# Optimization experiments

Measured on AMD Instinct MI355X. Metric: run time of the kernel, lower is better.

Reference implementation:

```python
import jax, jax.numpy as jnp
import numpy as np

B, C, H, W = 2, 3, 256, 256
K_STEPS = 50
RHO = 0.5
SIGMA_INIT = float(0.5 / np.sqrt(2.0 * C))  # sigma_init == tau_init = 0.5/sqrt(C*2)


def nabla(x):
    # forward finite differences, zero at last row/col. x: [B,C,H,W] -> [B,C,2,H,W]
    dh = jnp.pad(x[:, :, 1:, :] - x[:, :, :-1, :], ((0, 0), (0, 0), (0, 1), (0, 0)))
    dw = jnp.pad(x[:, :, :, 1:] - x[:, :, :, :-1], ((0, 0), (0, 0), (0, 0), (0, 1)))
    return jnp.stack([dh, dw], axis=2)


def nablaT(u):
    # adjoint of nabla (negative divergence). u: [B,C,2,H,W] -> [B,C,H,W]
    v0, v1 = u[:, :, 0], u[:, :, 1]
    out = jnp.zeros(v0.shape, v0.dtype)
    out = out.at[:, :, 1:, :].add(v0[:, :, :-1, :]).at[:, :, :-1, :].add(-v0[:, :, :-1, :])
    out = out.at[:, :, :, 1:].add(v1[:, :, :, :-1]).at[:, :, :, :-1].add(-v1[:, :, :, :-1])
    return out


def l12_prox_conjugate(v, lamb):
    # Moreau: prox_{sigma*(lamb*f)*}(v) = v - sigma*prox_{(lamb/sigma) f}(v/sigma)
    # which for L12 reduces to projection onto the lamb-ball per group.
    # groups: l2 over axes (1,-2,-1) = (C,H,W), one group per (B, F).
    norm = jnp.sqrt(jnp.sum(v * v, axis=(1, 3, 4), keepdims=True))
    scale = lamb / jnp.maximum(norm, lamb)  # == min(1, lamb/norm), safe at 0
    return v * scale


def l2_prox(z, y, gamma):
    # argmin_u 0.5||u-z||^2 + gamma*0.5||u-y||^2  (A = identity)
    return (z + gamma * y) / (1.0 + gamma)


def setup_inputs() -> dict:
    key = jax.random.key(0)
    y = jax.random.normal(key, (B, C, H, W), dtype=jnp.float32)
    lambd = jnp.float32(-1.0)  # learnable scalar log-regularization weight
    return {"y": y, "lambd": lambd}


def reference(y, lambd):
    elambda = jnp.exp(lambd)
    # set_init: A_dagger = identity
    x0 = y
    xt0 = jnp.zeros_like(x0)
    u0 = nabla(x0)

    def step(carry, _):
        x, xt, u, sigma, tau = carry
        u_next = l12_prox_conjugate(u + sigma * nabla(xt), elambda)
        x_next = l2_prox(x - tau * nablaT(u_next), y, tau)
        chi = 1.0 / jnp.sqrt(1.0 + 2.0 * RHO * tau)
        tau_next = tau * chi
        sigma_next = sigma / chi
        xt_next = (1.0 + chi) * x_next - chi * x
        return (x_next, xt_next, u_next, sigma_next, tau_next), None

    init = (x0, xt0, u0, jnp.float32(SIGMA_INIT), jnp.float32(SIGMA_INIT))
    (x, xt, u, _, _), _ = jax.lax.scan(step, init, None, length=K_STEPS)
    return (x, xt, u)
```

## Files before the change

### kernel.cpp

```cpp
#include <hip/hip_runtime.h>
#include <math.h>

constexpr int Cc = 3, Hh = 256;
constexpr int NX = 393216;
constexpr int R = 8;
constexpr int NBLK = 192;
constexpr int KSTEPS = 50;
constexpr int ROWQ = 128;
constexpr int BROWS = 12;
constexpr int SLOTQ = NBLK * BROWS * ROWQ;

using u64 = unsigned long long;
constexpr u64 SENT = 0x8000000080000000ull;

__device__ __forceinline__ float4 ld4(const float* p, int i) { return ((const float4*)p)[i]; }
__device__ __forceinline__ void st4(float* p, int i, float4 v) { ((float4*)p)[i] = v; }
__device__ __forceinline__ float4 mk4(float a, float b, float c, float d) { return make_float4(a, b, c, d); }
__device__ __forceinline__ u64 ldq(const u64* p) {
    return __hip_atomic_load(p, __ATOMIC_RELAXED, __HIP_MEMORY_SCOPE_AGENT);
}
__device__ __forceinline__ void stq(u64* p, u64 v) {
    __hip_atomic_store(p, v, __ATOMIC_RELAXED, __HIP_MEMORY_SCOPE_AGENT);
}
__device__ __forceinline__ void pub4(u64* w, float4 v) {
    union { float f[2]; u64 q; } a, b;
    a.f[0] = v.x; a.f[1] = v.y; b.f[0] = v.z; b.f[1] = v.w;
    stq(w, a.q); stq(w + 1, b.q);
}
__device__ __forceinline__ float4 unp(u64 lo, u64 hi) {
    union { u64 q; float f[2]; } a, b; a.q = lo; b.q = hi;
    return make_float4(a.f[0], a.f[1], b.f[0], b.f[1]);
}
__device__ __forceinline__ float4 col3(float4 P, float4 A, float4 B, float a, float b) {
    return mk4(fmaf(a, A.x, fmaf(b, B.x, P.x)), fmaf(a, A.y, fmaf(b, B.y, P.y)),
               fmaf(a, A.z, fmaf(b, B.z, P.z)), fmaf(a, A.w, fmaf(b, B.w, P.w)));
}
__device__ __forceinline__ float4 f4sub(float4 a, float4 b) {
    return mk4(a.x - b.x, a.y - b.y, a.z - b.z, a.w - b.w);
}
__device__ __forceinline__ float4 f4s(float4 a, float s) {
    return mk4(a.x * s, a.y * s, a.z * s, a.w * s);
}
__device__ __forceinline__ float4 f4fma(float s, float4 a, float4 b) {
    return mk4(fmaf(s, a.x, b.x), fmaf(s, a.y, b.y), fmaf(s, a.z, b.z), fmaf(s, a.w, b.w));
}
__device__ __forceinline__ float4 nth(float4 vm, bool up, float4 v0x, bool dn) {
    return mk4((up ? vm.x : 0.f) - (dn ? v0x.x : 0.f), (up ? vm.y : 0.f) - (dn ? v0x.y : 0.f),
               (up ? vm.z : 0.f) - (dn ? v0x.z : 0.f), (up ? vm.w : 0.f) - (dn ? v0x.w : 0.f));
}
__device__ __forceinline__ float4 ntw(float4 v1x, int c4) {
    float ul = __shfl_up(v1x.w, 1, 64);
    return mk4(((c4 > 0) ? ul : 0.f) - v1x.x, v1x.x - v1x.y, v1x.y - v1x.z,
               v1x.z - ((c4 < 63) ? v1x.w : 0.f));
}
__device__ __forceinline__ float4 gradw(float4 t, int c4) {
    float xn = __shfl_down(t.x, 1, 64);
    return mk4(t.y - t.x, t.z - t.y, t.w - t.z, (c4 < 63) ? (xn - t.w) : 0.f);
}
__device__ __forceinline__ void barld() {
    asm volatile("s_waitcnt lgkmcnt(0)" ::: "memory");
    __builtin_amdgcn_sched_barrier(0);
    __builtin_amdgcn_s_barrier();
    __builtin_amdgcn_sched_barrier(0);
}

__global__ void init_ws(u64* h0, u64* h1, u64* h2, u64* parts) {
    int i = blockIdx.x * 256 + threadIdx.x;
    if (i < SLOTQ) { h0[i] = SENT; h1[i] = SENT; h2[i] = SENT; }
    if (i < (KSTEPS + 1) * NBLK) parts[i] = SENT;
}

__global__ void __launch_bounds__(512, 1) cp_persist(
    const float* __restrict__ y, const float* __restrict__ lambd,
    float* __restrict__ xout, float* __restrict__ xtout, float* __restrict__ uout,
    u64* __restrict__ h0, u64* __restrict__ h1, u64* __restrict__ h2,
    u64* __restrict__ parts)
{
    __shared__ float sv0[8 * 256];
    __shared__ float sxtP[9 * 256];
    __shared__ float sxtA[9 * 256];
    __shared__ float sxtB[9 * 256];
    __shared__ float2 pw[8];

    const int tid = threadIdx.x, blk = blockIdx.x;
    const int bc = blk >> 5, tile = blk & 31, r0 = tile * R;
    const int c4 = tid & 63, trow = tid >> 6;
    const int b = (bc >= Cc) ? 1 : 0;
    const float lamb = expf(lambd[0]);
    const int gh = r0 + trow;
    const int j4 = bc * 16384 + gh * 64 + c4;

    float4 yv, xcur, v0c, v1c;
    float4 xpP, xpA, xpB, p0P, p0A, p0B, p1P, p1A, p1B;
    float4 yh = mk4(0, 0, 0, 0), vmtop = yh, v0h = yh, v1h = yh, xoh = yh;

    float tau = 0.20412414523193150818f;
    float sig = tau;
    float chi = 0.f, sigs = 0.f;
    float alpha = 0.f, beta = 0.f;

    auto slotp = [&](int r) -> u64* { return (r == 0) ? h0 : ((r == 1) ? h1 : h2); };

    auto wavesum2 = [&](float& a, float& bb) {
        #pragma unroll
        for (int m = 1; m < 64; m <<= 1) { a += __shfl_xor(a, m, 64); bb += __shfl_xor(bb, m, 64); }
    };

    auto pollscale = [&](int s) {
        const u64* pb = parts + (size_t)s * NBLK + b * 96;
        const int i1 = 64 + (c4 & 31);
        u64 q0, q1;
        for (;;) {
            q0 = ldq(pb + c4);
            q1 = ldq(pb + i1);
            if (__all((q0 != SENT) && (q1 != SENT))) break;
            __builtin_amdgcn_s_sleep(1);
        }
        asm volatile("" ::: "memory");
        union { u64 q; float f[2]; } a;
        a.q = q0;
        float g0 = a.f[0], g1 = a.f[1];
        a.q = q1;
        if (c4 < 32) { g0 += a.f[0]; g1 += a.f[1]; }
        wavesum2(g0, g1);
        alpha = lamb / fmaxf(sqrtf(g0), lamb);
        beta  = lamb / fmaxf(sqrtf(g1), lamb);
    };

    auto wavenorm = [&]() {
        float pa0 = v0c.x*v0c.x + v0c.y*v0c.y + v0c.z*v0c.z + v0c.w*v0c.w;
        float pa1 = v1c.x*v1c.x + v1c.y*v1c.y + v1c.z*v1c.z + v1c.w*v1c.w;
        wavesum2(pa0, pa1);
        if (c4 == 0) pw[trow] = make_float2(pa0, pa1);
    };
    auto pubparts = [&](int s) {
        if (tid == 0) {
            float q0 = 0.f, q1 = 0.f;
            #pragma unroll
            for (int w = 0; w < 8; ++w) { q0 += pw[w].x; q1 += pw[w].y; }
            union { float f[2]; u64 q; } pk; pk.f[0] = q0; pk.f[1] = q1;
            stq(parts + (size_t)s * NBLK + blk, pk.q);
        }
    };

    auto expand = [&](u64* hb, bool pub) {
        const float inv = 1.f / (1.f + tau);
        const float tin = tau * inv;
        const float opc = 1.f + chi;
        float4 xtP, xtA, xtB;
        {
            float4 vm = (trow > 0) ? ((float4*)(sv0 + (trow - 1) * 256))[c4] : vmtop;
            float4 NT0 = nth(vm, gh > 0, v0c, gh < Hh - 1);
            float4 NT1 = ntw(v1c, c4);
            float4 BASE = f4s(f4fma(tau, yv, xcur), inv);
            float4 xA = f4s(NT0, -tin);
            float4 xB = f4s(NT1, -tin);
            xpP = BASE; xpA = xA; xpB = xB;
            xtP = f4fma(-chi, xcur, f4s(BASE, opc));
            xtA = f4s(xA, opc);
            xtB = f4s(xB, opc);
            if (trow >= 1) {
                ((float4*)(sxtP + trow * 256))[c4] = xtP;
                ((float4*)(sxtA + trow * 256))[c4] = xtA;
                ((float4*)(sxtB + trow * 256))[c4] = xtB;
            }
            if (pub && trow == 0) {
                u64* rbase = hb + ((size_t)blk * BROWS) * ROWQ;
                pub4(rbase +  9 * ROWQ + 2 * c4, BASE);
                pub4(rbase + 10 * ROWQ + 2 * c4, xA);
                pub4(rbase + 11 * ROWQ + 2 * c4, xB);
            }
        }
        if (trow == 0 && tile < 31) {
            float4 vmh = ((float4*)(sv0 + 7 * 256))[c4];
            float4 NT0h = nth(vmh, true, v0h, true);
            float4 NT1h = ntw(v1h, c4);
            float4 BASEh = f4s(f4fma(tau, yh, xoh), inv);
            float4 xAh = f4s(NT0h, -tin);
            float4 xBh = f4s(NT1h, -tin);
            ((float4*)(sxtP + 8 * 256))[c4] = f4fma(-chi, xoh, f4s(BASEh, opc));
            ((float4*)(sxtA + 8 * 256))[c4] = f4s(xAh, opc);
            ((float4*)(sxtB + 8 * 256))[c4] = f4s(xBh, opc);
        }
        barld();
        {
            float4 dhP = mk4(0, 0, 0, 0), dhA = dhP, dhB = dhP;
            if (gh < Hh - 1) {
                dhP = f4sub(((float4*)(sxtP + (trow + 1) * 256))[c4], xtP);
                dhA = f4sub(((float4*)(sxtA + (trow + 1) * 256))[c4], xtA);
                dhB = f4sub(((float4*)(sxtB + (trow + 1) * 256))[c4], xtB);
            }
            float4 dwP = gradw(xtP, c4);
            float4 dwA = gradw(xtA, c4);
            float4 dwB = gradw(xtB, c4);
            p0P = f4s(dhP, sigs);
            p0A = f4fma(sigs, dhA, v0c);
            p0B = f4s(dhB, sigs);
            p1P = f4s(dwP, sigs);
            p1A = f4s(dwA, sigs);
            p1B = f4fma(sigs, dwB, v1c);
            if (pub) {
                u64* rbase = hb + ((size_t)blk * BROWS) * ROWQ;
                if (trow == 0) {
                    pub4(rbase + 3 * ROWQ + 2 * c4, p0P);
                    pub4(rbase + 4 * ROWQ + 2 * c4, p0A);
                    pub4(rbase + 5 * ROWQ + 2 * c4, p0B);
                    pub4(rbase + 6 * ROWQ + 2 * c4, p1P);
                    pub4(rbase + 7 * ROWQ + 2 * c4, p1A);
                    pub4(rbase + 8 * ROWQ + 2 * c4, p1B);
                }
                if (trow == 7) {
                    pub4(rbase + 0 * ROWQ + 2 * c4, p0P);
                    pub4(rbase + 1 * ROWQ + 2 * c4, p0A);
                    pub4(rbase + 2 * ROWQ + 2 * c4, p0B);
                }
            }
        }
        barld();
    };

    {
        yv = ld4(y, j4);
        xcur = yv;
        float4 dh = mk4(0, 0, 0, 0);
        if (gh < Hh - 1) dh = f4sub(ld4(y, j4 + 64), yv);
        v0c = dh;
        v1c = gradw(yv, c4);
        ((float4*)(sv0 + trow * 256))[c4] = v0c;
        if (trow == 0) {
            if (tile < 31) {
                const int j4h = bc * 16384 + (r0 + 8) * 64 + c4;
                yh = ld4(y, j4h);
                v0h = f4sub(ld4(y, j4h + 64), yh);
                v1h = gradw(yh, c4);
                xoh = yh;
            }
            if (tile > 0) {
                float4 ym = ld4(y, bc * 16384 + (r0 - 1) * 64 + c4);
                vmtop = f4sub(yv, ym);
            }
        }
        wavenorm();
        barld();
        pubparts(1);
        chi = 1.f / sqrtf(1.f + tau);
        sigs = sig / chi;
        expand(slotp(0), true);
        tau *= chi; sig = sigs;
    }

    for (int s = 1; s < KSTEPS; ++s) {
        pollscale(s);
        chi = 1.f / sqrtf(1.f + tau);
        sigs = sig / chi;

        xcur = col3(xpP, xpA, xpB, alpha, beta);
        v0c  = col3(p0P, p0A, p0B, alpha, beta);
        v1c  = col3(p1P, p1A, p1B, alpha, beta);
        ((float4*)(sv0 + trow * 256))[c4] = v0c;

        u64* hbp = slotp((s - 1) % 3);
        if (trow == 0) {
            if (tile > 0) {
                const u64* ra = hbp + ((size_t)(blk - 1) * BROWS) * ROWQ + 2 * c4;
                u64 a0, a1, a2, a3, a4, a5;
                for (;;) {
                    a0 = ldq(ra);            a1 = ldq(ra + 1);
                    a2 = ldq(ra + ROWQ);     a3 = ldq(ra + ROWQ + 1);
                    a4 = ldq(ra + 2 * ROWQ); a5 = ldq(ra + 2 * ROWQ + 1);
                    if (__all((a0 != SENT) && (a1 != SENT) && (a2 != SENT) &&
                              (a3 != SENT) && (a4 != SENT) && (a5 != SENT))) break;
                    __builtin_amdgcn_s_sleep(1);
                }
                vmtop = col3(unp(a0, a1), unp(a2, a3), unp(a4, a5), alpha, beta);
            }
            if (tile < 31) {
                const u64* rb = hbp + ((size_t)(blk + 1) * BROWS) * ROWQ + 2 * c4;
                u64 b0, b1, b2, b3, b4, b5, b6, b7, b8, b9, b10, b11, b12, b13, b14, b15, b16, b17;
                for (;;) {
                    b0  = ldq(rb + 3 * ROWQ);  b1  = ldq(rb + 3 * ROWQ + 1);
                    b2  = ldq(rb + 4 * ROWQ);  b3  = ldq(rb + 4 * ROWQ + 1);
                    b4  = ldq(rb + 5 * ROWQ);  b5  = ldq(rb + 5 * ROWQ + 1);
                    b6  = ldq(rb + 6 * ROWQ);  b7  = ldq(rb + 6 * ROWQ + 1);
                    b8  = ldq(rb + 7 * ROWQ);  b9  = ldq(rb + 7 * ROWQ + 1);
                    b10 = ldq(rb + 8 * ROWQ);  b11 = ldq(rb + 8 * ROWQ + 1);
                    b12 = ldq(rb + 9 * ROWQ);  b13 = ldq(rb + 9 * ROWQ + 1);
                    b14 = ldq(rb + 10 * ROWQ); b15 = ldq(rb + 10 * ROWQ + 1);
                    b16 = ldq(rb + 11 * ROWQ); b17 = ldq(rb + 11 * ROWQ + 1);
                    bool ok = (b0 != SENT) && (b1 != SENT) && (b2 != SENT) && (b3 != SENT) &&
                              (b4 != SENT) && (b5 != SENT) && (b6 != SENT) && (b7 != SENT) &&
                              (b8 != SENT) && (b9 != SENT) && (b10 != SENT) && (b11 != SENT) &&
                              (b12 != SENT) && (b13 != SENT) && (b14 != SENT) && (b15 != SENT) &&
                              (b16 != SENT) && (b17 != SENT);
                    if (__all(ok)) break;
                    __builtin_amdgcn_s_sleep(1);
                }
                v0h = col3(unp(b0, b1),   unp(b2, b3),   unp(b4, b5),   alpha, beta);
                v1h = col3(unp(b6, b7),   unp(b8, b9),   unp(b10, b11), alpha, beta);
                xoh = col3(unp(b12, b13), unp(b14, b15), unp(b16, b17), alpha, beta);
            }
        }
        asm volatile("" ::: "memory");

        if (s <= 47) {
            u64* rb2 = slotp((s + 1) % 3) + ((size_t)blk * BROWS) * ROWQ;
            if (trow == 0) {
                #pragma unroll
                for (int r = 3; r < 12; ++r) {
                    stq(rb2 + r * ROWQ + 2 * c4, SENT);
                    stq(rb2 + r * ROWQ + 2 * c4 + 1, SENT);
                }
            } else if (trow == 7) {
                #pragma unroll
                for (int r = 0; r < 3; ++r) {
                    stq(rb2 + r * ROWQ + 2 * c4, SENT);
                    stq(rb2 + r * ROWQ + 2 * c4 + 1, SENT);
                }
            }
        }
        wavenorm();
        barld();
        pubparts(s + 1);
        expand(slotp(s % 3), s < KSTEPS - 1);
        tau *= chi; sig = sigs;
    }

    pollscale(KSTEPS);
    const float opc = 1.f + chi;
    const int iv4 = bc * 32768 + gh * 64 + c4;
    float4 xf_ = col3(xpP, xpA, xpB, alpha, beta);
    float4 xtf = f4fma(-chi, xcur, f4s(xf_, opc));
    st4(xout, j4, xf_);
    st4(xtout, j4, xtf);
    st4(uout, iv4, f4s(v0c, alpha));
    st4(uout, iv4 + 16384, f4s(v1c, beta));
}

extern "C" void kernel_launch(void* const* d_in, const int* in_sizes, int n_in,
                              void* d_out, int out_size, void* d_ws, size_t ws_size,
                              hipStream_t stream) {
    (void)in_sizes; (void)n_in; (void)out_size; (void)ws_size;
    const float* y     = (const float*)d_in[0];
    const float* lambd = (const float*)d_in[1];
    float* xout  = (float*)d_out;
    float* xtout = xout + NX;
    float* uout  = xout + 2 * NX;

    u64* h0 = (u64*)d_out;
    u64* h1 = h0 + SLOTQ;
    u64* h2 = (u64*)d_ws;
    u64* parts = h2 + SLOTQ;

    init_ws<<<SLOTQ / 256, 256, 0, stream>>>(h0, h1, h2, parts);
    cp_persist<<<NBLK, 512, 0, stream>>>(y, lambd, xout, xtout, uout, h0, h1, h2, parts);
}
```

Before: 208.5 us.

## Move parts and halo polling to end of step and peel final iteration

Waiting for the global norm partials and for neighbour halos now happens at the end of each step, right after expand, instead of at the start of the next step. Only the halo-reading wave polls for halos, and the other waves can clear the next slot's sentinels before the norm-dependent scaling. The last step is peeled so the final expand skips the gradient and publish work that nothing reads, and it computes the outputs directly. This reorders cross-block synchronisation within the persistent kernel, which risks changing stall behaviour and correctness subtleties.

```diff
diff --git a/kernel.cpp b/kernel.cpp
--- a/kernel.cpp
+++ b/kernel.cpp
@@ -57,6 +57,9 @@
     float xn = __shfl_down(t.x, 1, 64);
     return mk4(t.y - t.x, t.z - t.y, t.w - t.z, (c4 < 63) ? (xn - t.w) : 0.f);
 }
+__device__ __forceinline__ float dot4(float4 a, float4 b) {
+    return a.x * b.x + a.y * b.y + a.z * b.z + a.w * b.w;
+}
 __device__ __forceinline__ void barld() {
     asm volatile("s_waitcnt lgkmcnt(0)" ::: "memory");
     __builtin_amdgcn_sched_barrier(0);
@@ -77,9 +80,7 @@
     u64* __restrict__ parts)
 {
     __shared__ float sv0[8 * 256];
-    __shared__ float sxtP[9 * 256];
-    __shared__ float sxtA[9 * 256];
-    __shared__ float sxtB[9 * 256];
+    __shared__ float sxtP[9 * 256], sxtA[9 * 256], sxtB[9 * 256];
     __shared__ float2 pw[8];
 
     const int tid = threadIdx.x, blk = blockIdx.x;
@@ -93,20 +94,16 @@
     float4 yv, xcur, v0c, v1c;
     float4 xpP, xpA, xpB, p0P, p0A, p0B, p1P, p1A, p1B;
     float4 yh = mk4(0, 0, 0, 0), vmtop = yh, v0h = yh, v1h = yh, xoh = yh;
-
-    float tau = 0.20412414523193150818f;
-    float sig = tau;
-    float chi = 0.f, sigs = 0.f;
-    float alpha = 0.f, beta = 0.f;
+    float tau = 0.20412414523193150818f, sig = tau, chi = 0.f, sigs = 0.f;
+    float g0 = 0.f, g1 = 0.f;
 
     auto slotp = [&](int r) -> u64* { return (r == 0) ? h0 : ((r == 1) ? h1 : h2); };
-
     auto wavesum2 = [&](float& a, float& bb) {
         #pragma unroll
         for (int m = 1; m < 64; m <<= 1) { a += __shfl_xor(a, m, 64); bb += __shfl_xor(bb, m, 64); }
     };
 
-    auto pollscale = [&](int s) {
+    auto pollparts = [&](int s) {
         const u64* pb = parts + (size_t)s * NBLK + b * 96;
         const int i1 = 64 + (c4 & 31);
         u64 q0, q1;
@@ -119,17 +116,55 @@
         asm volatile("" ::: "memory");
         union { u64 q; float f[2]; } a;
         a.q = q0;
-        float g0 = a.f[0], g1 = a.f[1];
+        g0 = a.f[0]; g1 = a.f[1];
         a.q = q1;
         if (c4 < 32) { g0 += a.f[0]; g1 += a.f[1]; }
         wavesum2(g0, g1);
-        alpha = lamb / fmaxf(sqrtf(g0), lamb);
-        beta  = lamb / fmaxf(sqrtf(g1), lamb);
-    };
-
+    };
+    auto halopoll = [&](int sl, float al, float be) {
+        u64* hbp = slotp(sl);
+        if (tile > 0) {
+            const u64* ra = hbp + ((size_t)(blk - 1) * BROWS) * ROWQ + 2 * c4;
+            u64 a0, a1, a2, a3, a4, a5;
+            for (;;) {
+                a0 = ldq(ra);            a1 = ldq(ra + 1);
+                a2 = ldq(ra + ROWQ);     a3 = ldq(ra + ROWQ + 1);
+                a4 = ldq(ra + 2 * ROWQ); a5 = ldq(ra + 2 * ROWQ + 1);
+                if (__all((a0 != SENT) && (a1 != SENT) && (a2 != SENT) &&
+                          (a3 != SENT) && (a4 != SENT) && (a5 != SENT))) break;
+                __builtin_amdgcn_s_sleep(1);
+            }
+            vmtop = col3(unp(a0, a1), unp(a2, a3), unp(a4, a5), al, be);
+        } else vmtop = mk4(0, 0, 0, 0);
+        if (tile < 31) {
+            const u64* rb = hbp + ((size_t)(blk + 1) * BROWS) * ROWQ + 2 * c4;
+            u64 b0, b1, b2, b3, b4, b5, b6, b7, b8, b9, b10, b11, b12, b13, b14, b15, b16, b17;
+            for (;;) {
+                b0  = ldq(rb + 3 * ROWQ);  b1  = ldq(rb + 3 * ROWQ + 1);
+                b2  = ldq(rb + 4 * ROWQ);  b3  = ldq(rb + 4 * ROWQ + 1);
+                b4  = ldq(rb + 5 * ROWQ);  b5  = ldq(rb + 5 * ROWQ + 1);
+                b6  = ldq(rb + 6 * ROWQ);  b7  = ldq(rb + 6 * ROWQ + 1);
+                b8  = ldq(rb + 7 * ROWQ);  b9  = ldq(rb + 7 * ROWQ + 1);
+                b10 = ldq(rb + 8 * ROWQ);  b11 = ldq(rb + 8 * ROWQ + 1);
+                b12 = ldq(rb + 9 * ROWQ);  b13 = ldq(rb + 9 * ROWQ + 1);
+                b14 = ldq(rb + 10 * ROWQ); b15 = ldq(rb + 10 * ROWQ + 1);
+                b16 = ldq(rb + 11 * ROWQ); b17 = ldq(rb + 11 * ROWQ + 1);
+                bool ok = (b0 != SENT) && (b1 != SENT) && (b2 != SENT) && (b3 != SENT) &&
+                          (b4 != SENT) && (b5 != SENT) && (b6 != SENT) && (b7 != SENT) &&
+                          (b8 != SENT) && (b9 != SENT) && (b10 != SENT) && (b11 != SENT) &&
+                          (b12 != SENT) && (b13 != SENT) && (b14 != SENT) && (b15 != SENT) &&
+                          (b16 != SENT) && (b17 != SENT);
+                if (__all(ok)) break;
+                __builtin_amdgcn_s_sleep(1);
+            }
+            v0h = col3(unp(b0, b1),   unp(b2, b3),   unp(b4, b5),   al, be);
+            v1h = col3(unp(b6, b7),   unp(b8, b9),   unp(b10, b11), al, be);
+            xoh = col3(unp(b12, b13), unp(b14, b15), unp(b16, b17), al, be);
+        }
+        asm volatile("" ::: "memory");
+    };
     auto wavenorm = [&]() {
-        float pa0 = v0c.x*v0c.x + v0c.y*v0c.y + v0c.z*v0c.z + v0c.w*v0c.w;
-        float pa1 = v1c.x*v1c.x + v1c.y*v1c.y + v1c.z*v1c.z + v1c.w*v1c.w;
+        float pa0 = dot4(v0c, v0c), pa1 = dot4(v1c, v1c);
         wavesum2(pa0, pa1);
         if (c4 == 0) pw[trow] = make_float2(pa0, pa1);
     };
@@ -142,19 +177,15 @@
             stq(parts + (size_t)s * NBLK + blk, pk.q);
         }
     };
-
     auto expand = [&](u64* hb, bool pub) {
-        const float inv = 1.f / (1.f + tau);
-        const float tin = tau * inv;
-        const float opc = 1.f + chi;
+        const float inv = 1.f / (1.f + tau), tin = tau * inv, opc = 1.f + chi;
         float4 xtP, xtA, xtB;
         {
             float4 vm = (trow > 0) ? ((float4*)(sv0 + (trow - 1) * 256))[c4] : vmtop;
             float4 NT0 = nth(vm, gh > 0, v0c, gh < Hh - 1);
             float4 NT1 = ntw(v1c, c4);
             float4 BASE = f4s(f4fma(tau, yv, xcur), inv);
-            float4 xA = f4s(NT0, -tin);
-            float4 xB = f4s(NT1, -tin);
+            float4 xA = f4s(NT0, -tin), xB = f4s(NT1, -tin);
             xpP = BASE; xpA = xA; xpB = xB;
             xtP = f4fma(-chi, xcur, f4s(BASE, opc));
             xtA = f4s(xA, opc);
@@ -176,44 +207,33 @@
             float4 NT0h = nth(vmh, true, v0h, true);
             float4 NT1h = ntw(v1h, c4);
             float4 BASEh = f4s(f4fma(tau, yh, xoh), inv);
-            float4 xAh = f4s(NT0h, -tin);
-            float4 xBh = f4s(NT1h, -tin);
             ((float4*)(sxtP + 8 * 256))[c4] = f4fma(-chi, xoh, f4s(BASEh, opc));
-            ((float4*)(sxtA + 8 * 256))[c4] = f4s(xAh, opc);
-            ((float4*)(sxtB + 8 * 256))[c4] = f4s(xBh, opc);
-        }
-        barld();
-        {
-            float4 dhP = mk4(0, 0, 0, 0), dhA = dhP, dhB = dhP;
-            if (gh < Hh - 1) {
-                dhP = f4sub(((float4*)(sxtP + (trow + 1) * 256))[c4], xtP);
-                dhA = f4sub(((float4*)(sxtA + (trow + 1) * 256))[c4], xtA);
-                dhB = f4sub(((float4*)(sxtB + (trow + 1) * 256))[c4], xtB);
-            }
-            float4 dwP = gradw(xtP, c4);
-            float4 dwA = gradw(xtA, c4);
-            float4 dwB = gradw(xtB, c4);
-            p0P = f4s(dhP, sigs);
-            p0A = f4fma(sigs, dhA, v0c);
-            p0B = f4s(dhB, sigs);
-            p1P = f4s(dwP, sigs);
-            p1A = f4s(dwA, sigs);
-            p1B = f4fma(sigs, dwB, v1c);
-            if (pub) {
-                u64* rbase = hb + ((size_t)blk * BROWS) * ROWQ;
-                if (trow == 0) {
-                    pub4(rbase + 3 * ROWQ + 2 * c4, p0P);
-                    pub4(rbase + 4 * ROWQ + 2 * c4, p0A);
-                    pub4(rbase + 5 * ROWQ + 2 * c4, p0B);
-                    pub4(rbase + 6 * ROWQ + 2 * c4, p1P);
-                    pub4(rbase + 7 * ROWQ + 2 * c4, p1A);
-                    pub4(rbase + 8 * ROWQ + 2 * c4, p1B);
-                }
-                if (trow == 7) {
-                    pub4(rbase + 0 * ROWQ + 2 * c4, p0P);
-                    pub4(rbase + 1 * ROWQ + 2 * c4, p0A);
-                    pub4(rbase + 2 * ROWQ + 2 * c4, p0B);
-                }
+            ((float4*)(sxtA + 8 * 256))[c4] = f4s(f4s(NT0h, -tin), opc);
+            ((float4*)(sxtB + 8 * 256))[c4] = f4s(f4s(NT1h, -tin), opc);
+        }
+        barld();
+        float4 dhP = mk4(0, 0, 0, 0), dhA = dhP, dhB = dhP;
+        if (gh < Hh - 1) {
+            dhP = f4sub(((float4*)(sxtP + (trow + 1) * 256))[c4], xtP);
+            dhA = f4sub(((float4*)(sxtA + (trow + 1) * 256))[c4], xtA);
+            dhB = f4sub(((float4*)(sxtB + (trow + 1) * 256))[c4], xtB);
+        }
+        float4 dwP = gradw(xtP, c4), dwA = gradw(xtA, c4), dwB = gradw(xtB, c4);
+        p0P = f4s(dhP, sigs); p0A = f4fma(sigs, dhA, v0c); p0B = f4s(dhB, sigs);
+        p1P = f4s(dwP, sigs); p1A = f4s(dwA, sigs); p1B = f4fma(sigs, dwB, v1c);
+        if (pub) {
+            u64* rbase = hb + ((size_t)blk * BROWS) * ROWQ;
+            if (trow == 0) {
+                pub4(rbase + 3 * ROWQ + 2 * c4, p0P);
+                pub4(rbase + 4 * ROWQ + 2 * c4, p0A);
+                pub4(rbase + 5 * ROWQ + 2 * c4, p0B);
+                pub4(rbase + 6 * ROWQ + 2 * c4, p1P);
+                pub4(rbase + 7 * ROWQ + 2 * c4, p1A);
+                pub4(rbase + 8 * ROWQ + 2 * c4, p1B);
+            } else if (trow == 7) {
+                pub4(rbase + 0 * ROWQ + 2 * c4, p0P);
+                pub4(rbase + 1 * ROWQ + 2 * c4, p0A);
+                pub4(rbase + 2 * ROWQ + 2 * c4, p0B);
             }
         }
         barld();
@@ -222,9 +242,7 @@
     {
         yv = ld4(y, j4);
         xcur = yv;
-        float4 dh = mk4(0, 0, 0, 0);
-        if (gh < Hh - 1) dh = f4sub(ld4(y, j4 + 64), yv);
-        v0c = dh;
+        v0c = (gh < Hh - 1) ? f4sub(ld4(y, j4 + 64), yv) : mk4(0, 0, 0, 0);
         v1c = gradw(yv, c4);
         ((float4*)(sv0 + trow * 256))[c4] = v0c;
         if (trow == 0) {
@@ -241,68 +259,26 @@
             }
         }
         wavenorm();
-        barld();
-        pubparts(1);
         chi = 1.f / sqrtf(1.f + tau);
         sigs = sig / chi;
+        barld();
+        pubparts(1);
         expand(slotp(0), true);
+        pollparts(1);
+        if (trow == 0) {
+            float al = lamb / fmaxf(sqrtf(g0), lamb);
+            float be = lamb / fmaxf(sqrtf(g1), lamb);
+            halopoll(0, al, be);
+        }
         tau *= chi; sig = sigs;
     }
 
-    for (int s = 1; s < KSTEPS; ++s) {
-        pollscale(s);
+    for (int s = 1; s < KSTEPS - 1; ++s) {
+        const float al = lamb / fmaxf(sqrtf(g0), lamb);
+        const float be = lamb / fmaxf(sqrtf(g1), lamb);
         chi = 1.f / sqrtf(1.f + tau);
         sigs = sig / chi;
-
-        xcur = col3(xpP, xpA, xpB, alpha, beta);
-        v0c  = col3(p0P, p0A, p0B, alpha, beta);
-        v1c  = col3(p1P, p1A, p1B, alpha, beta);
-        ((float4*)(sv0 + trow * 256))[c4] = v0c;
-
-        u64* hbp = slotp((s - 1) % 3);
-        if (trow == 0) {
-            if (tile > 0) {
-                const u64* ra = hbp + ((size_t)(blk - 1) * BROWS) * ROWQ + 2 * c4;
-                u64 a0, a1, a2, a3, a4, a5;
-                for (;;) {
-                    a0 = ldq(ra);            a1 = ldq(ra + 1);
-                    a2 = ldq(ra + ROWQ);     a3 = ldq(ra + ROWQ + 1);
-                    a4 = ldq(ra + 2 * ROWQ); a5 = ldq(ra + 2 * ROWQ + 1);
-                    if (__all((a0 != SENT) && (a1 != SENT) && (a2 != SENT) &&
-                              (a3 != SENT) && (a4 != SENT) && (a5 != SENT))) break;
-                    __builtin_amdgcn_s_sleep(1);
-                }
-                vmtop = col3(unp(a0, a1), unp(a2, a3), unp(a4, a5), alpha, beta);
-            }
-            if (tile < 31) {
-                const u64* rb = hbp + ((size_t)(blk + 1) * BROWS) * ROWQ + 2 * c4;
-                u64 b0, b1, b2, b3, b4, b5, b6, b7, b8, b9, b10, b11, b12, b13, b14, b15, b16, b17;
-                for (;;) {
-                    b0  = ldq(rb + 3 * ROWQ);  b1  = ldq(rb + 3 * ROWQ + 1);
-                    b2  = ldq(rb + 4 * ROWQ);  b3  = ldq(rb + 4 * ROWQ + 1);
-                    b4  = ldq(rb + 5 * ROWQ);  b5  = ldq(rb + 5 * ROWQ + 1);
-                    b6  = ldq(rb + 6 * ROWQ);  b7  = ldq(rb + 6 * ROWQ + 1);
-                    b8  = ldq(rb + 7 * ROWQ);  b9  = ldq(rb + 7 * ROWQ + 1);
-                    b10 = ldq(rb + 8 * ROWQ);  b11 = ldq(rb + 8 * ROWQ + 1);
-                    b12 = ldq(rb + 9 * ROWQ);  b13 = ldq(rb + 9 * ROWQ + 1);
-                    b14 = ldq(rb + 10 * ROWQ); b15 = ldq(rb + 10 * ROWQ + 1);
-                    b16 = ldq(rb + 11 * ROWQ); b17 = ldq(rb + 11 * ROWQ + 1);
-                    bool ok = (b0 != SENT) && (b1 != SENT) && (b2 != SENT) && (b3 != SENT) &&
-                              (b4 != SENT) && (b5 != SENT) && (b6 != SENT) && (b7 != SENT) &&
-                              (b8 != SENT) && (b9 != SENT) && (b10 != SENT) && (b11 != SENT) &&
-                              (b12 != SENT) && (b13 != SENT) && (b14 != SENT) && (b15 != SENT) &&
-                              (b16 != SENT) && (b17 != SENT);
-                    if (__all(ok)) break;
-                    __builtin_amdgcn_s_sleep(1);
-                }
-                v0h = col3(unp(b0, b1),   unp(b2, b3),   unp(b4, b5),   alpha, beta);
-                v1h = col3(unp(b6, b7),   unp(b8, b9),   unp(b10, b11), alpha, beta);
-                xoh = col3(unp(b12, b13), unp(b14, b15), unp(b16, b17), alpha, beta);
-            }
-        }
-        asm volatile("" ::: "memory");
-
-        if (s <= 47) {
+        {
             u64* rb2 = slotp((s + 1) % 3) + ((size_t)blk * BROWS) * ROWQ;
             if (trow == 0) {
                 #pragma unroll
@@ -318,22 +294,51 @@
                 }
             }
         }
+        xcur = col3(xpP, xpA, xpB, al, be);
+        v0c  = col3(p0P, p0A, p0B, al, be);
+        v1c  = col3(p1P, p1A, p1B, al, be);
+        ((float4*)(sv0 + trow * 256))[c4] = v0c;
         wavenorm();
         barld();
         pubparts(s + 1);
-        expand(slotp(s % 3), s < KSTEPS - 1);
+        expand(slotp(s % 3), true);
+        pollparts(s + 1);
+        if (trow == 0) {
+            float al2 = lamb / fmaxf(sqrtf(g0), lamb);
+            float be2 = lamb / fmaxf(sqrtf(g1), lamb);
+            halopoll(s % 3, al2, be2);
+        }
         tau *= chi; sig = sigs;
     }
 
-    pollscale(KSTEPS);
-    const float opc = 1.f + chi;
-    const int iv4 = bc * 32768 + gh * 64 + c4;
-    float4 xf_ = col3(xpP, xpA, xpB, alpha, beta);
-    float4 xtf = f4fma(-chi, xcur, f4s(xf_, opc));
-    st4(xout, j4, xf_);
-    st4(xtout, j4, xtf);
-    st4(uout, iv4, f4s(v0c, alpha));
-    st4(uout, iv4 + 16384, f4s(v1c, beta));
+    {
+        const float al = lamb / fmaxf(sqrtf(g0), lamb);
+        const float be = lamb / fmaxf(sqrtf(g1), lamb);
+        chi = 1.f / sqrtf(1.f + tau);
+        xcur = col3(xpP, xpA, xpB, al, be);
+        v0c  = col3(p0P, p0A, p0B, al, be);
+        v1c  = col3(p1P, p1A, p1B, al, be);
+        ((float4*)(sv0 + trow * 256))[c4] = v0c;
+        wavenorm();
+        barld();
+        pubparts(KSTEPS);
+        const float inv = 1.f / (1.f + tau), tin = tau * inv;
+        float4 vm = (trow > 0) ? ((float4*)(sv0 + (trow - 1) * 256))[c4] : vmtop;
+        float4 NT0 = nth(vm, gh > 0, v0c, gh < Hh - 1);
+        float4 NT1 = ntw(v1c, c4);
+        float4 BASE = f4s(f4fma(tau, yv, xcur), inv);
+        float4 xA = f4s(NT0, -tin), xB = f4s(NT1, -tin);
+        pollparts(KSTEPS);
+        const float a50 = lamb / fmaxf(sqrtf(g0), lamb);
+        const float b50 = lamb / fmaxf(sqrtf(g1), lamb);
+        float4 x50 = col3(BASE, xA, xB, a50, b50);
+        float4 xt50 = f4fma(-chi, xcur, f4s(x50, 1.f + chi));
+        const int iv4 = bc * 32768 + gh * 64 + c4;
+        st4(xout, j4, x50);
+        st4(xtout, j4, xt50);
+        st4(uout, iv4, f4s(v0c, a50));
+        st4(uout, iv4 + 16384, f4s(v1c, b50));
+    }
 }
 
 extern "C" void kernel_launch(void* const* d_in, const int* in_sizes, int n_in,
```

After: 216.6 us. +3.9%, slower.
